# Performance work log

Hardware: AMD Instinct MI355X
Metric: run time of the kernel (lower is better)

The kernel has to match this reference:

```python
import jax, jax.numpy as jnp
import numpy as np

NUM_HEADS = 16


def _local_attn(q, k, v, bias, nq, nk):
    """Blocked local attention, faithful to rearrange_to_dense_trunk semantics.
    q,k,v: [B,H,N,D]; bias: [B,Hb,N,N] (Hb broadcasts against H).
    Trunk i (queries [i*nq,(i+1)*nq)) attends keys at original indices
    [i*nq - pad_left, i*nq - pad_left + nk); out-of-range keys/values/bias are
    zero-padded (the module pads with zeros, no -inf key masking).
    Assumes N % nq == 0 (q_pad_length == 0, so the query mask loop is a no-op).
    """
    B, H, N, D = q.shape
    T = N // nq                      # n_trunks
    pad_left = (nk - nq) // 2
    Lp = (T - 1) * nq + nk           # padded key length so every window is full
    pad_right = Lp - pad_left - N
    k_p = jnp.pad(k, ((0, 0), (0, 0), (pad_left, pad_right), (0, 0)))
    v_p = jnp.pad(v, ((0, 0), (0, 0), (pad_left, pad_right), (0, 0)))
    b_p = jnp.pad(bias, ((0, 0), (0, 0), (0, 0), (pad_left, pad_right)))
    # window gather indices: [T, nk]
    kidx = jnp.arange(T)[:, None] * nq + jnp.arange(nk)[None, :]
    k_t = k_p[:, :, kidx, :]         # [B,H,T,nk,D]
    v_t = v_p[:, :, kidx, :]         # [B,H,T,nk,D]
    Bb, Hb = bias.shape[0], bias.shape[1]
    b_r = b_p.reshape(Bb, Hb, T, nq, Lp)
    b_t = jnp.take_along_axis(b_r, kidx[None, None, :, None, :], axis=-1)  # [Bb,Hb,T,nq,nk]
    q_t = q.reshape(B, H, T, nq, D)
    scores = jnp.einsum('bhtqd,bhtkd->bhtqk', q_t, k_t) + b_t
    w = jax.nn.softmax(scores, axis=-1)
    o = jnp.einsum('bhtqk,bhtkd->bhtqd', w, v_t)
    return o.reshape(B, H, N, D)


def setup_inputs() -> dict:
    key = jax.random.key(0)
    ks = jax.random.split(key, 8)
    B, N, C = 1, 4096, 256
    H, D = NUM_HEADS, 64
    HD = H * D
    q_x = jax.random.normal(ks[0], (B, N, C), dtype=jnp.float32)
    kv_x = jax.random.normal(ks[1], (B, N, C), dtype=jnp.float32)
    attn_bias = jax.random.normal(ks[2], (B, 1, N, N), dtype=jnp.float32) * 0.1
    Wq = jax.random.normal(ks[3], (C, HD), dtype=jnp.float32) / np.sqrt(C).astype(np.float32)
    Wk = jax.random.normal(ks[4], (C, HD), dtype=jnp.float32) / np.sqrt(C).astype(np.float32)
    Wv = jax.random.normal(ks[5], (C, HD), dtype=jnp.float32) / np.sqrt(C).astype(np.float32)
    Wg = jax.random.normal(ks[6], (C, HD), dtype=jnp.float32) / np.sqrt(C).astype(np.float32)
    Wo = jax.random.normal(ks[7], (HD, C), dtype=jnp.float32) / np.sqrt(HD).astype(np.float32)
    return {"q_x": q_x, "kv_x": kv_x, "attn_bias": attn_bias,
            "Wq": Wq, "Wk": Wk, "Wv": Wv, "Wg": Wg, "Wo": Wo,
            "n_queries": 64, "n_keys": 256}


def reference(q_x, kv_x, attn_bias, Wq, Wk, Wv, Wg, Wo, n_queries, n_keys):
    B, N, C = q_x.shape
    H = NUM_HEADS
    D = Wq.shape[-1] // H
    def split_heads(x):
        return x.reshape(B, N, H, D).transpose(0, 2, 1, 3)  # [B,H,N,D]
    q = split_heads(q_x @ Wq) / jnp.sqrt(jnp.float32(D))
    k = split_heads(kv_x @ Wk)
    v = split_heads(kv_x @ Wv)
    o = _local_attn(q, k, v, attn_bias, n_queries, n_keys)
    o = o.transpose(0, 2, 1, 3).reshape(B, N, H * D)
    g = jax.nn.sigmoid(q_x @ Wg)  # gating head
    return (o * g) @ Wo
```

## Files before the change

kernel.cpp:

```cpp
#include <hip/hip_runtime.h>

#define N_ 4096
#define C_ 256
#define H_ 16
#define D_ 64
#define HD_ 1024

typedef __attribute__((ext_vector_type(8))) __bf16 bf16x8;
typedef __attribute__((ext_vector_type(8))) _Float16 f16x8;
typedef __attribute__((ext_vector_type(4))) _Float16 f16x4;
typedef __attribute__((ext_vector_type(4))) float f32x4;

__device__ __forceinline__ void gload16(const void* g, void* l) {
    __builtin_amdgcn_global_load_lds(
        (const __attribute__((address_space(1))) unsigned int*)g,
        (__attribute__((address_space(3))) unsigned int*)l, 16, 0, 0);
}

__global__ __launch_bounds__(256) void convert_kernel(
    const float* __restrict__ q_x, const float* __restrict__ kv_x,
    const float* __restrict__ Wq, const float* __restrict__ Wk,
    const float* __restrict__ Wv, const float* __restrict__ Wg,
    const float* __restrict__ Wo,
    _Float16* __restrict__ Xf, _Float16* __restrict__ WTf,
    _Float16* __restrict__ WoTf)
{
    __shared__ float ts[64][65];
    const int b = blockIdx.x;
    const int tid = threadIdx.x;

    if (b < 512) {
        const int seg = b >> 8;
        const float* src = seg ? kv_x : q_x;
        _Float16* df = Xf + (size_t)seg * 1048576;
        const int base = (b & 255) * 4096 + tid * 16;
#pragma unroll
        for (int q = 0; q < 4; ++q) {
            float4 v = *(const float4*)&src[base + q * 4];
            f16x4 fv;
            fv[0] = (_Float16)v.x; fv[1] = (_Float16)v.y;
            fv[2] = (_Float16)v.z; fv[3] = (_Float16)v.w;
            *(f16x4*)&df[base + q * 4] = fv;
        }
        return;
    }

    const float* src;
    _Float16* df;
    int srcC, dstC, r0, c0;
    if (b < 768) {
        const int widx = (b - 512) >> 6;
        const int tile = (b - 512) & 63;
        src = (widx == 0) ? Wq : (widx == 1) ? Wk : (widx == 2) ? Wv : Wg;
        df = WTf + (size_t)widx * 262144;
        srcC = 1024; dstC = 256;
        r0 = (tile >> 4) * 64;
        c0 = (tile & 15) * 64;
    } else {
        const int tile = b - 768;
        src = Wo; df = WoTf;
        srcC = 256; dstC = 1024;
        r0 = (tile >> 2) * 64;
        c0 = (tile & 3) * 64;
    }
    {
        const int r = tid >> 2;
        const int cch = (tid & 3) * 16;
#pragma unroll
        for (int q = 0; q < 4; ++q) {
            float4 v = *(const float4*)&src[(size_t)(r0 + r) * srcC + c0 + cch + q * 4];
            ts[r][cch + q * 4 + 0] = v.x;
            ts[r][cch + q * 4 + 1] = v.y;
            ts[r][cch + q * 4 + 2] = v.z;
            ts[r][cch + q * 4 + 3] = v.w;
        }
    }
    __syncthreads();
    {
        const int c = tid >> 2;
        const int rch = (tid & 3) * 16;
#pragma unroll
        for (int q = 0; q < 4; ++q) {
            f16x4 fv;
#pragma unroll
            for (int j = 0; j < 4; ++j)
                fv[j] = (_Float16)ts[rch + q * 4 + j][c];
            *(f16x4*)&df[(size_t)(c0 + c) * dstC + r0 + rch + q * 4] = fv;
        }
    }
}

__global__ __launch_bounds__(256) void proj_mfma(
    const _Float16* __restrict__ Xf, const _Float16* __restrict__ WTf,
    _Float16* __restrict__ qh, _Float16* __restrict__ kh,
    _Float16* __restrict__ vh, _Float16* __restrict__ gh)
{
    __shared__ __align__(16) char psmem[34816];
    _Float16* As = (_Float16*)psmem;
    _Float16* Bs = (_Float16*)(psmem + 16384);

    const int lb  = blockIdx.x;
    const int xcd = lb & 7;
    const int gr  = (lb >> 6) * 8 + xcd;
    const int g   = gr >> 5;
    const int m0  = (gr & 31) * 128;
    const int c0  = ((lb >> 3) & 7) * 128;

    const _Float16* A = Xf + ((g == 1 || g == 2) ? 1048576 : 0);
    const _Float16* B = WTf + (size_t)g * 262144;

    const int tid  = threadIdx.x;
    const int wave = tid >> 6;
    const int lane = tid & 63;
    const int wr   = wave >> 1;
    const int wc   = wave & 1;
    const int frow = lane & 15;
    const int grp  = lane >> 4;

    f32x4 acc[4][4];
#pragma unroll
    for (int i = 0; i < 4; ++i)
#pragma unroll
        for (int j = 0; j < 4; ++j) acc[i][j] = (f32x4){0.f, 0.f, 0.f, 0.f};

    const int srow = tid >> 3;
    const int sch  = tid & 7;

    for (int kt = 0; kt < 256; kt += 64) {
        __syncthreads();
#pragma unroll
        for (int p = 0; p < 4; ++p) {
            const int row = p * 32 + srow;
            const int koff = kt + ((sch ^ (row & 7)) << 3);
            gload16(A + (size_t)(m0 + row) * 256 + koff, (char*)As + p * 4096 + tid * 16);
            gload16(B + (size_t)(c0 + row) * 256 + koff, (char*)Bs + p * 4096 + tid * 16);
        }
        __syncthreads();

#pragma unroll
        for (int ks = 0; ks < 2; ++ks) {
            f16x8 af[4], bf[4];
#pragma unroll
            for (int f = 0; f < 4; ++f) {
                const int ra = wr * 64 + f * 16 + frow;
                const int rb = wc * 64 + f * 16 + frow;
                af[f] = *(const f16x8*)((char*)As + ra * 128 + (((ks * 4 + grp) ^ (ra & 7)) << 4));
                bf[f] = *(const f16x8*)((char*)Bs + rb * 128 + (((ks * 4 + grp) ^ (rb & 7)) << 4));
            }
#pragma unroll
            for (int i = 0; i < 4; ++i)
#pragma unroll
                for (int j = 0; j < 4; ++j)
                    acc[i][j] = __builtin_amdgcn_mfma_f32_16x16x32_f16(af[i], bf[j], acc[i][j], 0, 0, 0);
        }
    }

    __syncthreads();
    _Float16* Epi = (_Float16*)psmem;
    {
        const float scale = (g == 0) ? 0.125f : 1.f;
#pragma unroll
        for (int i = 0; i < 4; ++i)
#pragma unroll
            for (int j = 0; j < 4; ++j) {
                const int rr = wr * 64 + i * 16 + grp * 4;
                const int cc = wc * 64 + j * 16 + frow;
#pragma unroll
                for (int v = 0; v < 4; ++v) {
                    float x = acc[i][j][v];
                    x = (g == 3) ? 1.f / (1.f + __expf(-x)) : x * scale;
                    Epi[(rr + v) * 136 + cc] = (_Float16)x;
                }
            }
    }
    __syncthreads();
    {
        const int ch   = tid & 15;
        const int head = ch >> 3;
        const int e8   = (ch & 7) * 8;
#pragma unroll
        for (int p = 0; p < 8; ++p) {
            const int r = p * 16 + (tid >> 4);
            const f16x8 val = *(const f16x8*)&Epi[r * 136 + head * 64 + e8];
            if (g == 3) {
                *(f16x8*)&gh[(size_t)(m0 + r) * HD_ + c0 + head * 64 + e8] = val;
            } else {
                _Float16* dst = (g == 0) ? qh : (g == 1) ? kh : vh;
                const int hh = (c0 >> 6) + head;
                *(f16x8*)&dst[((size_t)hh * N_ + m0 + r) * D_ + e8] = val;
            }
        }
    }
}

__global__ __launch_bounds__(256, 4) void attn_mfma(
    const _Float16* __restrict__ qh, const _Float16* __restrict__ kh,
    const _Float16* __restrict__ vh, const float* __restrict__ bias,
    const _Float16* __restrict__ gh, _Float16* __restrict__ of)
{
    __shared__ __align__(16) char smem[34816];
    _Float16* Qs = (_Float16*)smem;
    char* Ks = smem + 8192;
    _Float16* Ps = (_Float16*)smem;
    _Float16* Vs = (_Float16*)(smem + 17408);
    float* Oe = (float*)smem;

    const int lb  = blockIdx.x;
    const int xcd = lb & 7;
    const int j_  = lb >> 3;
    const int h   = j_ >> 3;
    const int t   = xcd * 8 + (j_ & 7);
    const int tid = threadIdx.x;
    const int lane = tid & 63;
    const int wv = tid >> 6;
    const int frow = lane & 15;
    const int grp = lane >> 4;
    const int kbase = t * 64 - 96;

    const char* qbase = (const char*)qh + (size_t)(h * N_ + t * 64) * 128;
    const char* kbase_p = (const char*)kh + (size_t)h * N_ * 128;

#pragma unroll
    for (int q = 0; q < 2; ++q) {
        const int lin = q * 4096 + tid * 16;
        const int row = lin >> 7;
        const int ch = (lin >> 4) & 7;
        gload16(qbase + row * 128 + ((ch ^ (row & 7)) << 4), (char*)Qs + lin);
    }

    f32x4 sacc[16];

#pragma unroll
    for (int p = 0; p < 2; ++p) {
#pragma unroll
        for (int q = 0; q < 4; ++q) {
            const int lin = q * 4096 + tid * 16;
            const int row = lin >> 7;
            const int ch = (lin >> 4) & 7;
            const int kg = kbase + p * 128 + row;
            if ((unsigned)kg < (unsigned)N_) {
                gload16(kbase_p + (size_t)kg * 128 + ((ch ^ (row & 7)) << 4), Ks + lin);
            } else {
                *(float4*)(Ks + lin) = make_float4(0.f, 0.f, 0.f, 0.f);
            }
        }
        {
            const int rowg = t * 64 + wv * 16 + grp * 4;
#pragma unroll
            for (int j = 0; j < 8; ++j) {
                const int colg = kbase + p * 128 + j * 16 + frow;
                const bool ok = (unsigned)colg < (unsigned)N_;
#pragma unroll
                for (int v = 0; v < 4; ++v)
                    sacc[p * 8 + j][v] = ok ? bias[(size_t)(rowg + v) * N_ + colg] : 0.f;
            }
        }
        __syncthreads();
        const int rq = wv * 16 + frow;
#pragma unroll
        for (int ks = 0; ks < 2; ++ks) {
            const f16x8 aq = *(const f16x8*)((char*)Qs + rq * 128 + (((ks * 4 + grp) ^ (rq & 7)) << 4));
#pragma unroll
            for (int j = 0; j < 8; ++j) {
                const int rk = j * 16 + frow;
                const f16x8 bk = *(const f16x8*)(Ks + rk * 128 + (((ks * 4 + grp) ^ (rk & 7)) << 4));
                sacc[p * 8 + j] = __builtin_amdgcn_mfma_f32_16x16x32_f16(aq, bk, sacc[p * 8 + j], 0, 0, 0);
            }
        }
        __syncthreads();
    }

    float inv[4];
#pragma unroll
    for (int v = 0; v < 4; ++v) {
        float m = sacc[0][v];
#pragma unroll
        for (int f = 1; f < 16; ++f) m = fmaxf(m, sacc[f][v]);
        m = fmaxf(m, __shfl_xor(m, 1));
        m = fmaxf(m, __shfl_xor(m, 2));
        m = fmaxf(m, __shfl_xor(m, 4));
        m = fmaxf(m, __shfl_xor(m, 8));
        float l = 0.f;
#pragma unroll
        for (int f = 0; f < 16; ++f) {
            float e = __expf(sacc[f][v] - m);
            sacc[f][v] = e;
            l += e;
        }
        l += __shfl_xor(l, 1);
        l += __shfl_xor(l, 2);
        l += __shfl_xor(l, 4);
        l += __shfl_xor(l, 8);
        inv[v] = 1.f / l;
    }

    f32x4 oacc[4];
#pragma unroll
    for (int jd = 0; jd < 4; ++jd) oacc[jd] = (f32x4){0.f, 0.f, 0.f, 0.f};

#pragma unroll
    for (int c = 0; c < 2; ++c) {
        {
            const int sl = tid >> 1;
            const int d0 = (tid & 1) * 32;
            const int kg = kbase + c * 128 + sl;
            f16x8 vv[4];
            if ((unsigned)kg < (unsigned)N_) {
                const f16x8* vp = (const f16x8*)(vh + ((size_t)h * N_ + kg) * D_ + d0);
#pragma unroll
                for (int q = 0; q < 4; ++q) vv[q] = vp[q];
            } else {
#pragma unroll
                for (int q = 0; q < 4; ++q)
#pragma unroll
                    for (int e = 0; e < 8; ++e) vv[q][e] = (_Float16)0.f;
            }
#pragma unroll
            for (int q = 0; q < 4; ++q)
#pragma unroll
                for (int e = 0; e < 8; ++e)
                    Vs[(d0 + q * 8 + e) * 136 + sl] = vv[q][e];
        }
        {
            const int rb = wv * 16 + grp * 4;
#pragma unroll
            for (int j = 0; j < 8; ++j) {
                const int col = j * 16 + frow;
#pragma unroll
                for (int v = 0; v < 4; ++v)
                    Ps[(rb + v) * 136 + col] = (_Float16)sacc[c * 8 + j][v];
            }
        }
        __syncthreads();
        const int rp = wv * 16 + frow;
#pragma unroll
        for (int ks = 0; ks < 4; ++ks) {
            const f16x8 ap = *(const f16x8*)((char*)Ps + rp * 272 + ks * 64 + grp * 16);
#pragma unroll
            for (int jd = 0; jd < 4; ++jd) {
                const f16x8 bv = *(const f16x8*)((char*)Vs + (jd * 16 + frow) * 272 + ks * 64 + grp * 16);
                oacc[jd] = __builtin_amdgcn_mfma_f32_16x16x32_f16(ap, bv, oacc[jd], 0, 0, 0);
            }
        }
        __syncthreads();
    }

#pragma unroll
    for (int jd = 0; jd < 4; ++jd) {
        const int dcol = jd * 16 + frow;
#pragma unroll
        for (int v = 0; v < 4; ++v) {
            const int rn = wv * 16 + grp * 4 + v;
            Oe[rn * 68 + dcol] = oacc[jd][v] * inv[v];
        }
    }
    __syncthreads();
    {
        const int r   = tid >> 2;
        const int seg = tid & 3;
        const int n   = t * 64 + r;
        const int cg0 = h * 64 + seg * 16;
        const float* orow = &Oe[r * 68 + seg * 16];
        f32x4 o0 = *(const f32x4*)&orow[0];
        f32x4 o1 = *(const f32x4*)&orow[4];
        f32x4 o2 = *(const f32x4*)&orow[8];
        f32x4 o3 = *(const f32x4*)&orow[12];
        const f16x8 g0 = *(const f16x8*)&gh[(size_t)n * HD_ + cg0];
        const f16x8 g1 = *(const f16x8*)&gh[(size_t)n * HD_ + cg0 + 8];
        f16x8 r0, r1;
#pragma unroll
        for (int e = 0; e < 4; ++e) {
            r0[e]     = (_Float16)(o0[e] * (float)g0[e]);
            r0[4 + e] = (_Float16)(o1[e] * (float)g0[4 + e]);
            r1[e]     = (_Float16)(o2[e] * (float)g1[e]);
            r1[4 + e] = (_Float16)(o3[e] * (float)g1[4 + e]);
        }
        *(f16x8*)&of[(size_t)n * HD_ + cg0]     = r0;
        *(f16x8*)&of[(size_t)n * HD_ + cg0 + 8] = r1;
    }
}

__global__ __launch_bounds__(256) void out_mfma(
    const _Float16* __restrict__ of, const _Float16* __restrict__ WoTf,
    float* __restrict__ out)
{
    __shared__ __align__(16) _Float16 smem[2 * 4096];
    _Float16* As = smem;
    _Float16* Bs = smem + 4096;

    const int lb  = blockIdx.x;
    const int xcd = lb & 7;
    const int idx = lb >> 3;
    const int rowg = (idx >> 2) * 8 + xcd;
    const int m0  = rowg * 64;
    const int c0  = (idx & 3) * 64;

    const int tid  = threadIdx.x;
    const int wave = tid >> 6;
    const int lane = tid & 63;
    const int wr   = wave >> 1;
    const int wc   = wave & 1;
    const int frow = lane & 15;
    const int grp  = lane >> 4;

    f32x4 acc[2][2];
#pragma unroll
    for (int i = 0; i < 2; ++i)
#pragma unroll
        for (int j = 0; j < 2; ++j) acc[i][j] = (f32x4){0.f, 0.f, 0.f, 0.f};

    for (int kt = 0; kt < 1024; kt += 64) {
        __syncthreads();
#pragma unroll
        for (int p = 0; p < 2; ++p) {
            const int lin = p * 4096 + tid * 16;
            const int row = lin >> 7;
            const int ch  = (lin >> 4) & 7;
            const int koff = kt + ((ch ^ (row & 7)) << 3);
            gload16(of   + (size_t)(m0 + row) * HD_ + koff, (char*)As + lin);
            gload16(WoTf + (size_t)(c0 + row) * HD_ + koff, (char*)Bs + lin);
        }
        __syncthreads();

#pragma unroll
        for (int ks = 0; ks < 2; ++ks) {
            f16x8 af[2], bf[2];
#pragma unroll
            for (int f = 0; f < 2; ++f) {
                const int ra = wr * 32 + f * 16 + frow;
                const int rb = wc * 32 + f * 16 + frow;
                af[f] = *(const f16x8*)((char*)As + ra * 128 + (((ks * 4 + grp) ^ (ra & 7)) << 4));
                bf[f] = *(const f16x8*)((char*)Bs + rb * 128 + (((ks * 4 + grp) ^ (rb & 7)) << 4));
            }
#pragma unroll
            for (int i = 0; i < 2; ++i)
#pragma unroll
                for (int j = 0; j < 2; ++j)
                    acc[i][j] = __builtin_amdgcn_mfma_f32_16x16x32_f16(af[i], bf[j], acc[i][j], 0, 0, 0);
        }
    }

    const int rbase = grp * 4;
#pragma unroll
    for (int i = 0; i < 2; ++i)
#pragma unroll
        for (int j = 0; j < 2; ++j) {
            const int c = c0 + wc * 32 + j * 16 + frow;
#pragma unroll
            for (int v = 0; v < 4; ++v) {
                const int n = m0 + wr * 32 + i * 16 + rbase + v;
                out[(size_t)n * C_ + c] = acc[i][j][v];
            }
        }
}

extern "C" void kernel_launch(void* const* d_in, const int* in_sizes, int n_in,
                              void* d_out, int out_size, void* d_ws, size_t ws_size,
                              hipStream_t stream)
{
    const float* q_x  = (const float*)d_in[0];
    const float* kv_x = (const float*)d_in[1];
    const float* bias = (const float*)d_in[2];
    const float* Wq   = (const float*)d_in[3];
    const float* Wk   = (const float*)d_in[4];
    const float* Wv   = (const float*)d_in[5];
    const float* Wg   = (const float*)d_in[6];
    const float* Wo   = (const float*)d_in[7];
    float* out = (float*)d_out;

    char* ws = (char*)d_ws;
    const size_t MB = 1048576;
    _Float16* qh   = (_Float16*)(ws);
    _Float16* kh   = (_Float16*)(ws + 8  * MB);
    _Float16* vh   = (_Float16*)(ws + 16 * MB);
    _Float16* gh   = (_Float16*)(ws + 24 * MB);
    _Float16* of   = (_Float16*)(ws + 32 * MB);
    _Float16* Xf   = (_Float16*)(ws + 40 * MB);
    _Float16* WTf  = (_Float16*)(ws + 44 * MB);
    _Float16* WoTf = (_Float16*)(ws + 46 * MB);

    convert_kernel<<<832, 256, 0, stream>>>(q_x, kv_x, Wq, Wk, Wv, Wg, Wo,
                                            Xf, WTf, WoTf);
    proj_mfma<<<1024, 256, 0, stream>>>(Xf, WTf, qh, kh, vh, gh);
    attn_mfma<<<1024, 256, 0, stream>>>(qh, kh, vh, bias, gh, of);
    out_mfma<<<256, 256, 0, stream>>>(of, WoTf, out);
}
```

Measured before the change: 163.7 us.

## Load full key window at once in attention; halve out-projection row tile

The attention kernel now loads all 256 key rows and the full bias tile up front with a single barrier, instead of two 128-key passes each bracketed by syncs. This enlarges shared memory to 40 KB and issues more loads in flight. The output projection kernel moves from 64-row to 32-row tiles and doubles its grid from 256 to 512 blocks, so it fills more CUs on this hardware, at the cost of reloading the Wo tile more often. Both changes target latency and occupancy rather than arithmetic.

```diff
diff --git a/kernel.cpp b/kernel.cpp
--- a/kernel.cpp
+++ b/kernel.cpp
@@ -6,7 +6,6 @@
 #define D_ 64
 #define HD_ 1024
 
-typedef __attribute__((ext_vector_type(8))) __bf16 bf16x8;
 typedef __attribute__((ext_vector_type(8))) _Float16 f16x8;
 typedef __attribute__((ext_vector_type(4))) _Float16 f16x4;
 typedef __attribute__((ext_vector_type(4))) float f32x4;
@@ -198,7 +197,7 @@
     const _Float16* __restrict__ vh, const float* __restrict__ bias,
     const _Float16* __restrict__ gh, _Float16* __restrict__ of)
 {
-    __shared__ __align__(16) char smem[34816];
+    __shared__ __align__(16) char smem[40960];
     _Float16* Qs = (_Float16*)smem;
     char* Ks = smem + 8192;
     _Float16* Ps = (_Float16*)smem;
@@ -227,48 +226,47 @@
         const int ch = (lin >> 4) & 7;
         gload16(qbase + row * 128 + ((ch ^ (row & 7)) << 4), (char*)Qs + lin);
     }
+#pragma unroll
+    for (int q = 0; q < 8; ++q) {
+        const int lin = q * 4096 + tid * 16;
+        const int row = lin >> 7;
+        const int ch = (lin >> 4) & 7;
+        const int kg = kbase + row;
+        if ((unsigned)kg < (unsigned)N_) {
+            gload16(kbase_p + (size_t)kg * 128 + ((ch ^ (row & 7)) << 4), Ks + lin);
+        } else {
+            *(float4*)(Ks + lin) = make_float4(0.f, 0.f, 0.f, 0.f);
+        }
+    }
 
     f32x4 sacc[16];
-
-#pragma unroll
-    for (int p = 0; p < 2; ++p) {
-#pragma unroll
-        for (int q = 0; q < 4; ++q) {
-            const int lin = q * 4096 + tid * 16;
-            const int row = lin >> 7;
-            const int ch = (lin >> 4) & 7;
-            const int kg = kbase + p * 128 + row;
-            if ((unsigned)kg < (unsigned)N_) {
-                gload16(kbase_p + (size_t)kg * 128 + ((ch ^ (row & 7)) << 4), Ks + lin);
-            } else {
-                *(float4*)(Ks + lin) = make_float4(0.f, 0.f, 0.f, 0.f);
-            }
-        }
-        {
-            const int rowg = t * 64 + wv * 16 + grp * 4;
-#pragma unroll
-            for (int j = 0; j < 8; ++j) {
-                const int colg = kbase + p * 128 + j * 16 + frow;
-                const bool ok = (unsigned)colg < (unsigned)N_;
-#pragma unroll
-                for (int v = 0; v < 4; ++v)
-                    sacc[p * 8 + j][v] = ok ? bias[(size_t)(rowg + v) * N_ + colg] : 0.f;
-            }
-        }
-        __syncthreads();
+    {
+        const int rowg = t * 64 + wv * 16 + grp * 4;
+#pragma unroll
+        for (int j = 0; j < 16; ++j) {
+            const int colg = kbase + j * 16 + frow;
+            const bool ok = (unsigned)colg < (unsigned)N_;
+#pragma unroll
+            for (int v = 0; v < 4; ++v)
+                sacc[j][v] = ok ? bias[(size_t)(rowg + v) * N_ + colg] : 0.f;
+        }
+    }
+    __syncthreads();
+
+    {
         const int rq = wv * 16 + frow;
 #pragma unroll
         for (int ks = 0; ks < 2; ++ks) {
             const f16x8 aq = *(const f16x8*)((char*)Qs + rq * 128 + (((ks * 4 + grp) ^ (rq & 7)) << 4));
 #pragma unroll
-            for (int j = 0; j < 8; ++j) {
+            for (int j = 0; j < 16; ++j) {
                 const int rk = j * 16 + frow;
                 const f16x8 bk = *(const f16x8*)(Ks + rk * 128 + (((ks * 4 + grp) ^ (rk & 7)) << 4));
-                sacc[p * 8 + j] = __builtin_amdgcn_mfma_f32_16x16x32_f16(aq, bk, sacc[p * 8 + j], 0, 0, 0);
-            }
-        }
-        __syncthreads();
-    }
+                sacc[j] = __builtin_amdgcn_mfma_f32_16x16x32_f16(aq, bk, sacc[j], 0, 0, 0);
+            }
+        }
+    }
+    __syncthreads();
 
     float inv[4];
 #pragma unroll
@@ -384,16 +382,16 @@
     const _Float16* __restrict__ of, const _Float16* __restrict__ WoTf,
     float* __restrict__ out)
 {
-    __shared__ __align__(16) _Float16 smem[2 * 4096];
+    __shared__ __align__(16) _Float16 smem[2048 + 4096];
     _Float16* As = smem;
-    _Float16* Bs = smem + 4096;
+    _Float16* Bs = smem + 2048;
 
     const int lb  = blockIdx.x;
     const int xcd = lb & 7;
-    const int idx = lb >> 3;
-    const int rowg = (idx >> 2) * 8 + xcd;
-    const int m0  = rowg * 64;
-    const int c0  = (idx & 3) * 64;
+    const int s   = lb >> 3;
+    const int rowt = (s >> 2) * 8 + xcd;
+    const int m0  = rowt * 32;
+    const int c0  = (s & 3) * 64;
 
     const int tid  = threadIdx.x;
     const int wave = tid >> 6;
@@ -403,55 +401,51 @@
     const int frow = lane & 15;
     const int grp  = lane >> 4;
 
-    f32x4 acc[2][2];
-#pragma unroll
-    for (int i = 0; i < 2; ++i)
-#pragma unroll
-        for (int j = 0; j < 2; ++j) acc[i][j] = (f32x4){0.f, 0.f, 0.f, 0.f};
+    f32x4 acc[2];
+#pragma unroll
+    for (int j = 0; j < 2; ++j) acc[j] = (f32x4){0.f, 0.f, 0.f, 0.f};
 
     for (int kt = 0; kt < 1024; kt += 64) {
         __syncthreads();
+        {
+            const int row = tid >> 3;
+            const int ch  = tid & 7;
+            const int koff = kt + ((ch ^ (row & 7)) << 3);
+            gload16(of + (size_t)(m0 + row) * HD_ + koff, (char*)As + tid * 16);
+        }
 #pragma unroll
         for (int p = 0; p < 2; ++p) {
             const int lin = p * 4096 + tid * 16;
             const int row = lin >> 7;
             const int ch  = (lin >> 4) & 7;
             const int koff = kt + ((ch ^ (row & 7)) << 3);
-            gload16(of   + (size_t)(m0 + row) * HD_ + koff, (char*)As + lin);
             gload16(WoTf + (size_t)(c0 + row) * HD_ + koff, (char*)Bs + lin);
         }
         __syncthreads();
 
 #pragma unroll
         for (int ks = 0; ks < 2; ++ks) {
-            f16x8 af[2], bf[2];
-#pragma unroll
-            for (int f = 0; f < 2; ++f) {
-                const int ra = wr * 32 + f * 16 + frow;
-                const int rb = wc * 32 + f * 16 + frow;
-                af[f] = *(const f16x8*)((char*)As + ra * 128 + (((ks * 4 + grp) ^ (ra & 7)) << 4));
-                bf[f] = *(const f16x8*)((char*)Bs + rb * 128 + (((ks * 4 + grp) ^ (rb & 7)) << 4));
-            }
-#pragma unroll
-            for (int i = 0; i < 2; ++i)
-#pragma unroll
-                for (int j = 0; j < 2; ++j)
-                    acc[i][j] = __builtin_amdgcn_mfma_f32_16x16x32_f16(af[i], bf[j], acc[i][j], 0, 0, 0);
+            const int ra = wr * 16 + frow;
+            const f16x8 af = *(const f16x8*)((char*)As + ra * 128 + (((ks * 4 + grp) ^ (ra & 7)) << 4));
+#pragma unroll
+            for (int j = 0; j < 2; ++j) {
+                const int rb = wc * 32 + j * 16 + frow;
+                const f16x8 bf = *(const f16x8*)((char*)Bs + rb * 128 + (((ks * 4 + grp) ^ (rb & 7)) << 4));
+                acc[j] = __builtin_amdgcn_mfma_f32_16x16x32_f16(af, bf, acc[j], 0, 0, 0);
+            }
         }
     }
 
     const int rbase = grp * 4;
 #pragma unroll
-    for (int i = 0; i < 2; ++i)
-#pragma unroll
-        for (int j = 0; j < 2; ++j) {
-            const int c = c0 + wc * 32 + j * 16 + frow;
-#pragma unroll
-            for (int v = 0; v < 4; ++v) {
-                const int n = m0 + wr * 32 + i * 16 + rbase + v;
-                out[(size_t)n * C_ + c] = acc[i][j][v];
-            }
-        }
+    for (int j = 0; j < 2; ++j) {
+        const int c = c0 + wc * 32 + j * 16 + frow;
+#pragma unroll
+        for (int v = 0; v < 4; ++v) {
+            const int n = m0 + wr * 16 + rbase + v;
+            out[(size_t)n * C_ + c] = acc[j][v];
+        }
+    }
 }
 
 extern "C" void kernel_launch(void* const* d_in, const int* in_sizes, int n_in,
@@ -483,5 +477,5 @@
                                             Xf, WTf, WoTf);
     proj_mfma<<<1024, 256, 0, stream>>>(Xf, WTf, qh, kh, vh, gh);
     attn_mfma<<<1024, 256, 0, stream>>>(qh, kh, vh, bias, gh, of);
-    out_mfma<<<256, 256, 0, stream>>>(of, WoTf, out);
-}
+    out_mfma<<<512, 256, 0, stream>>>(of, WoTf, out);
+}
```

Measured after the change: 159.7 us. -2.4%, faster.
